# Performance work log

Hardware: AMD Instinct MI355X
Metric: run time of the kernel (lower is better)

## Reference

```python
import jax, jax.numpy as jnp
import numpy as np

N_NODES = 100000
N_EDGES = 1600000
DIMS = [128, 64, 64, 32]  # in -> hidden[0] -> hidden[1] -> out


def setup_inputs() -> dict:
    key = jax.random.key(0)
    ks = jax.random.split(key, 8)
    inp = {
        "features": jax.random.normal(ks[0], (N_NODES, DIMS[0]), dtype=jnp.float32),
        "edge_index": jax.random.randint(ks[1], (2, N_EDGES), 0, N_NODES, dtype=jnp.int32),
    }
    for i in range(3):
        # Glorot-ish init for the GCNConv linear weights; bias zeros (PyG default)
        inp[f"W{i}"] = jax.random.normal(ks[2 + i], (DIMS[i], DIMS[i + 1]), dtype=jnp.float32) / np.sqrt(DIMS[i]).astype(np.float32)
        inp[f"b{i}"] = jnp.zeros((DIMS[i + 1],), dtype=jnp.float32)
    return inp


def _gcn_conv(x, src, dst, norm, W, b, n):
    # PyG GCNConv: linear transform first, then normalized neighbor aggregation, then bias
    x = x @ W                                  # [n, d_out]
    msg = x[src] * norm[:, None]               # gather over edges (+ self loops)
    out = jax.ops.segment_sum(msg, dst, num_segments=n)
    return out + b


def reference(features, edge_index, W0, b0, W1, b1, W2, b2):
    n = features.shape[0]
    # add self loops (GCNConv default add_self_loops=True)
    loop = jnp.arange(n, dtype=edge_index.dtype)
    src = jnp.concatenate([edge_index[0], loop])
    dst = jnp.concatenate([edge_index[1], loop])
    # symmetric normalization: deg from destination (in-degree incl. self loops)
    deg = jax.ops.segment_sum(jnp.ones_like(dst, dtype=features.dtype), dst, num_segments=n)
    dis = jnp.where(deg > 0, jax.lax.rsqrt(jnp.maximum(deg, 1e-12)), 0.0)
    norm = dis[src] * dis[dst]                 # [E + n]

    x = jax.nn.relu(_gcn_conv(features, src, dst, norm, W0, b0, n))
    # dropout(p=0.2) treated as identity (deterministic inference reference)
    x = jax.nn.relu(_gcn_conv(x, src, dst, norm, W1, b1, n))
    x = _gcn_conv(x, src, dst, norm, W2, b2, n)  # last layer: no relu/dropout
    return x
```

## Files before the change

kernel.cpp:

```cpp
#include <hip/hip_runtime.h>
#include <hip/hip_fp16.h>

#define N_NODES 100000
#define N_EDGES 1600000
#define NPB 128
#define NBK ((N_NODES + NPB - 1) / NPB)
#define FBLK 256
#define EPB ((N_EDGES + FBLK - 1) / FBLK)
#define CAP 4096
#define SENT64 100000
#define SENT32 200000

typedef _Float16 h8 __attribute__((ext_vector_type(8)));
typedef float f4v __attribute__((ext_vector_type(4)));


__global__ void __launch_bounds__(256) hist_kernel(const int* __restrict__ dst, int* __restrict__ H) {
    __shared__ int h[NBK];
    for (int i = threadIdx.x; i < NBK; i += 256) h[i] = 0;
    __syncthreads();
    const int e0 = blockIdx.x * EPB;
    const int e1 = min(e0 + EPB, N_EDGES);
    for (int e = e0 + threadIdx.x; e < e1; e += 256) atomicAdd(&h[dst[e] >> 7], 1);
    __syncthreads();
    for (int i = threadIdx.x; i < NBK; i += 256) H[blockIdx.x * NBK + i] = h[i];
}


__global__ void __launch_bounds__(256) colscan_kernel(int* __restrict__ H, int* __restrict__ btot) {
    const int t = blockIdx.x * 256 + threadIdx.x;
    if (t >= NBK) return;
    int run = 0;
    for (int k = 0; k < FBLK; ++k) {
        int idx = k * NBK + t;
        int h = H[idx];
        H[idx] = run;
        run += h;
    }
    btot[t] = run;
}


__global__ void __launch_bounds__(1024) bucketscan_kernel(const int* __restrict__ btot,
                                                          int* __restrict__ bbase, int* __restrict__ bptr) {
    __shared__ int sh[1024];
    const int t = threadIdx.x;
    int v = (t < NBK) ? btot[t] : 0;
    sh[t] = v;
    __syncthreads();
    for (int off = 1; off < 1024; off <<= 1) {
        int u = (t >= off) ? sh[t - off] : 0;
        __syncthreads();
        sh[t] += u;
        __syncthreads();
    }
    if (t < NBK) { int e = sh[t] - v; bbase[t] = e; bptr[t] = e; }
    if (t == 0) bptr[NBK] = N_EDGES;
}


__global__ void __launch_bounds__(256) binfill_kernel(const int* __restrict__ src, const int* __restrict__ dst,
                                                      const int* __restrict__ H, const int* __restrict__ bbase,
                                                      int* __restrict__ tmp) {
    __shared__ int cur[NBK];
    const int k = blockIdx.x;
    for (int i = threadIdx.x; i < NBK; i += 256) cur[i] = H[k * NBK + i] + bbase[i];
    __syncthreads();
    const int e0 = k * EPB;
    const int e1 = min(e0 + EPB, N_EDGES);
    for (int e = e0 + threadIdx.x; e < e1; e += 256) {
        int s = src[e];
        int d = dst[e];
        int pos = atomicAdd(&cur[d >> 7], 1);
        tmp[pos] = s | ((d & (NPB - 1)) << 20);
    }
}


__global__ void __launch_bounds__(256) bucketfin_kernel(const int* __restrict__ tmp, const int* __restrict__ bptr,
                                                        int* __restrict__ esrc, int* __restrict__ rowptr,
                                                        float* __restrict__ dis, int n) {
    __shared__ int buf[CAP];
    __shared__ int cnt[NPB];
    __shared__ int sc[NPB];
    __shared__ int rp[NPB];
    __shared__ int fillc[NPB];
    const int b = blockIdx.x;
    const int d0 = b * NPB;
    const int nd = min(NPB, n - d0);
    const int base = bptr[b], end = bptr[b + 1];
    const int count = end - base;
    const int tid = threadIdx.x;

    for (int i = tid; i < NPB; i += 256) { cnt[i] = 0; fillc[i] = 0; }
    __syncthreads();
    for (int e = base + tid; e < end; e += 256) atomicAdd(&cnt[tmp[e] >> 20], 1);
    __syncthreads();

    if (tid < NPB) sc[tid] = cnt[tid];
    __syncthreads();
    for (int off = 1; off < NPB; off <<= 1) {
        int v = (tid < NPB && tid >= off) ? sc[tid - off] : 0;
        __syncthreads();
        if (tid < NPB) sc[tid] += v;
        __syncthreads();
    }
    if (tid < NPB) {
        int excl = sc[tid] - cnt[tid];
        rp[tid] = excl;
        if (tid < nd) {
            rowptr[d0 + tid] = base + excl;
            dis[d0 + tid] = rsqrtf((float)cnt[tid] + 1.0f);
        }
    }
    if (b == NBK - 1 && tid == 0) rowptr[n] = N_EDGES;
    __syncthreads();

    if (count <= CAP) {
        for (int t = base + tid; t < end; t += 256) {
            int w = tmp[t];
            int ld = w >> 20;
            int pos = rp[ld] + atomicAdd(&fillc[ld], 1);
            buf[pos] = w & 0xFFFFF;
        }
        __syncthreads();
        for (int t = tid; t < count; t += 256) esrc[base + t] = buf[t];
    } else {
        for (int t = base + tid; t < end; t += 256) {
            int w = tmp[t];
            int ld = w >> 20;
            int pos = rp[ld] + atomicAdd(&fillc[ld], 1);
            esrc[base + pos] = w & 0xFFFFF;
        }
    }
}


__global__ void transpose_all_kernel(const float* __restrict__ W0, const float* __restrict__ W1,
                                     const float* __restrict__ W2, __half* __restrict__ wt0,
                                     __half* __restrict__ wt1, __half* __restrict__ wt2,
                                     __half* __restrict__ ys) {
    int i = blockIdx.x * blockDim.x + threadIdx.x;
    if (i < 8192)       { int k = i / 64, c = i % 64;                 wt0[c * 128 + k] = __float2half(W0[i]); }
    else if (i < 12288) { int j = i - 8192;  int k = j / 64, c = j % 64; wt1[c * 64 + k] = __float2half(W1[j]); }
    else if (i < 14336) { int j = i - 12288; int k = j / 32, c = j % 32; wt2[c * 64 + k] = __float2half(W2[j]); }
    else if (i < 14368) { ((int*)(ys + (long)SENT64 * 64))[i - 14336] = 0; }
}


template <typename TIN, int DIN, int DOUT>
__global__ void __launch_bounds__(256) gemm_kernel(const TIN* __restrict__ x,
                                                   const __half* __restrict__ wt16,
                                                   const float* __restrict__ dis,
                                                   __half* __restrict__ ys, int n) {
    constexpr int WS = DIN + 8;
    constexpr int NT = DOUT / 16;
    constexpr int KC = DIN / 32;

    __shared__ _Float16 xls[64 * WS];
    __shared__ _Float16 wls[DOUT * WS];

    const int tid  = threadIdx.x;
    const int row0 = blockIdx.x * 64;

    for (int i = tid; i < DOUT * DIN / 8; i += 256) {
        int c = (i * 8) / DIN, k = (i * 8) % DIN;
        *(int4*)&wls[c * WS + k] = *(const int4*)&wt16[c * DIN + k];
    }
    if constexpr (sizeof(TIN) == 4) {
        for (int i = tid; i < 64 * DIN / 4; i += 256) {
            int r = (i * 4) / DIN, k = (i * 4) % DIN;
            float4 v = make_float4(0.f, 0.f, 0.f, 0.f);
            if (row0 + r < n) v = *(const float4*)&x[(long)(row0 + r) * DIN + k];
            _Float16 h[4] = {(_Float16)v.x, (_Float16)v.y, (_Float16)v.z, (_Float16)v.w};
            *(int2*)&xls[r * WS + k] = *(int2*)h;
        }
    } else {
        for (int i = tid; i < 64 * DIN / 8; i += 256) {
            int r = (i * 8) / DIN, k = (i * 8) % DIN;
            int4 v = make_int4(0, 0, 0, 0);
            if (row0 + r < n) v = *(const int4*)&x[(long)(row0 + r) * DIN + k];
            *(int4*)&xls[r * WS + k] = v;
        }
    }
    __syncthreads();

    const int wave = tid >> 6;
    const int lane = tid & 63;
    const int m16  = lane & 15;
    const int quad = lane >> 4;

    f4v acc[NT];
#pragma unroll
    for (int t = 0; t < NT; ++t) acc[t] = (f4v){0.f, 0.f, 0.f, 0.f};

    const int arow = wave * 16 + m16;
#pragma unroll
    for (int kc = 0; kc < KC; ++kc) {
        h8 a = *(const h8*)&xls[arow * WS + kc * 32 + quad * 8];
#pragma unroll
        for (int t = 0; t < NT; ++t) {
            h8 b = *(const h8*)&wls[(t * 16 + m16) * WS + kc * 32 + quad * 8];
            acc[t] = __builtin_amdgcn_mfma_f32_16x16x32_f16(a, b, acc[t], 0, 0, 0);
        }
    }

    float dsv[4];
    int   lrow[4];
#pragma unroll
    for (int reg = 0; reg < 4; ++reg) {
        lrow[reg] = wave * 16 + quad * 4 + reg;
        int grow  = row0 + lrow[reg];
        dsv[reg]  = (grow < n) ? dis[grow] : 0.f;
    }
    __syncthreads();
    _Float16* stage = xls;
#pragma unroll
    for (int t = 0; t < NT; ++t) {
#pragma unroll
        for (int reg = 0; reg < 4; ++reg)
            stage[lrow[reg] * DOUT + t * 16 + m16] = (_Float16)(acc[t][reg] * dsv[reg]);
    }
    __syncthreads();
    for (int i = tid; i < 64 * DOUT / 8; i += 256) {
        int off = i * 8;
        int r = off / DOUT;
        if (row0 + r < n)
            *(int4*)&ys[(long)row0 * DOUT + off] = *(int4*)&stage[off];
    }
}


__device__ __forceinline__ void acc8(int4 w, float* a) {
    __half2* h = (__half2*)&w;
    float2 f0 = __half22float2(h[0]);
    float2 f1 = __half22float2(h[1]);
    float2 f2 = __half22float2(h[2]);
    float2 f3 = __half22float2(h[3]);
    a[0] += f0.x; a[1] += f0.y; a[2] += f1.x; a[3] += f1.y;
    a[4] += f2.x; a[5] += f2.y; a[6] += f3.x; a[7] += f3.y;
}


__global__ void gather2h_kernel(const int* __restrict__ rowptr, const int* __restrict__ esrc,
                                const __half* __restrict__ ys, const float* __restrict__ dis,
                                const float* __restrict__ b, __half* __restrict__ out, int n) {
    const int node = blockIdx.x * 32 + (threadIdx.x >> 3);
    const int c = (threadIdx.x & 7) * 8;
    if (node >= n) return;

    float a[8];
    {
        int4 sw = *(const int4*)&ys[(long)node * 64 + c];
        __half2* h = (__half2*)&sw;
        float2 f0 = __half22float2(h[0]);
        float2 f1 = __half22float2(h[1]);
        float2 f2 = __half22float2(h[2]);
        float2 f3 = __half22float2(h[3]);
        a[0] = f0.x; a[1] = f0.y; a[2] = f1.x; a[3] = f1.y;
        a[4] = f2.x; a[5] = f2.y; a[6] = f3.x; a[7] = f3.y;
    }

    int k = rowptr[node];
    const int end = rowptr[node + 1];
    for (; k < end; k += 8) {
        int u0 = (k + 0 < end) ? esrc[k + 0] : SENT64;
        int u1 = (k + 1 < end) ? esrc[k + 1] : SENT64;
        int u2 = (k + 2 < end) ? esrc[k + 2] : SENT64;
        int u3 = (k + 3 < end) ? esrc[k + 3] : SENT64;
        int u4 = (k + 4 < end) ? esrc[k + 4] : SENT64;
        int u5 = (k + 5 < end) ? esrc[k + 5] : SENT64;
        int u6 = (k + 6 < end) ? esrc[k + 6] : SENT64;
        int u7 = (k + 7 < end) ? esrc[k + 7] : SENT64;
        int4 w0 = *(const int4*)&ys[(long)u0 * 64 + c];
        int4 w1 = *(const int4*)&ys[(long)u1 * 64 + c];
        int4 w2 = *(const int4*)&ys[(long)u2 * 64 + c];
        int4 w3 = *(const int4*)&ys[(long)u3 * 64 + c];
        int4 w4 = *(const int4*)&ys[(long)u4 * 64 + c];
        int4 w5 = *(const int4*)&ys[(long)u5 * 64 + c];
        int4 w6 = *(const int4*)&ys[(long)u6 * 64 + c];
        int4 w7 = *(const int4*)&ys[(long)u7 * 64 + c];
        acc8(w0, a); acc8(w1, a); acc8(w2, a); acc8(w3, a);
        acc8(w4, a); acc8(w5, a); acc8(w6, a); acc8(w7, a);
    }

    const float di = dis[node];
    __half hv[8];
#pragma unroll
    for (int j = 0; j < 8; ++j)
        hv[j] = __float2half(fmaxf(a[j] * di + b[c + j], 0.0f));
    *(int4*)&out[(long)node * 64 + c] = *(int4*)hv;
}


__global__ void gather4h_kernel(const int* __restrict__ rowptr, const int* __restrict__ esrc,
                                const __half* __restrict__ ys, const float* __restrict__ dis,
                                const float* __restrict__ b, float* __restrict__ out, int n) {
    const int node = blockIdx.x * 64 + (threadIdx.x >> 2);
    const int c = (threadIdx.x & 3) * 8;
    if (node >= n) return;

    float a[8];
    {
        int4 sw = *(const int4*)&ys[(long)node * 32 + c];
        __half2* h = (__half2*)&sw;
        float2 f0 = __half22float2(h[0]);
        float2 f1 = __half22float2(h[1]);
        float2 f2 = __half22float2(h[2]);
        float2 f3 = __half22float2(h[3]);
        a[0] = f0.x; a[1] = f0.y; a[2] = f1.x; a[3] = f1.y;
        a[4] = f2.x; a[5] = f2.y; a[6] = f3.x; a[7] = f3.y;
    }

    int k = rowptr[node];
    const int end = rowptr[node + 1];
    for (; k < end; k += 8) {
        int u0 = (k + 0 < end) ? esrc[k + 0] : SENT32;
        int u1 = (k + 1 < end) ? esrc[k + 1] : SENT32;
        int u2 = (k + 2 < end) ? esrc[k + 2] : SENT32;
        int u3 = (k + 3 < end) ? esrc[k + 3] : SENT32;
        int u4 = (k + 4 < end) ? esrc[k + 4] : SENT32;
        int u5 = (k + 5 < end) ? esrc[k + 5] : SENT32;
        int u6 = (k + 6 < end) ? esrc[k + 6] : SENT32;
        int u7 = (k + 7 < end) ? esrc[k + 7] : SENT32;
        int4 w0 = *(const int4*)&ys[(long)u0 * 32 + c];
        int4 w1 = *(const int4*)&ys[(long)u1 * 32 + c];
        int4 w2 = *(const int4*)&ys[(long)u2 * 32 + c];
        int4 w3 = *(const int4*)&ys[(long)u3 * 32 + c];
        int4 w4 = *(const int4*)&ys[(long)u4 * 32 + c];
        int4 w5 = *(const int4*)&ys[(long)u5 * 32 + c];
        int4 w6 = *(const int4*)&ys[(long)u6 * 32 + c];
        int4 w7 = *(const int4*)&ys[(long)u7 * 32 + c];
        acc8(w0, a); acc8(w1, a); acc8(w2, a); acc8(w3, a);
        acc8(w4, a); acc8(w5, a); acc8(w6, a); acc8(w7, a);
    }

    const float di = dis[node];
    float4 o0, o1;
    o0.x = a[0] * di + b[c + 0];
    o0.y = a[1] * di + b[c + 1];
    o0.z = a[2] * di + b[c + 2];
    o0.w = a[3] * di + b[c + 3];
    o1.x = a[4] * di + b[c + 4];
    o1.y = a[5] * di + b[c + 5];
    o1.z = a[6] * di + b[c + 6];
    o1.w = a[7] * di + b[c + 7];
    *(float4*)&out[(long)node * 32 + c] = o0;
    *(float4*)&out[(long)node * 32 + c + 4] = o1;
}


extern "C" void kernel_launch(void* const* d_in, const int* in_sizes, int n_in,
                              void* d_out, int out_size, void* d_ws, size_t ws_size,
                              hipStream_t stream) {
    const float* features = (const float*)d_in[0];
    const int*   ei       = (const int*)d_in[1];
    const float* W0 = (const float*)d_in[2];
    const float* b0 = (const float*)d_in[3];
    const float* W1 = (const float*)d_in[4];
    const float* b1 = (const float*)d_in[5];
    const float* W2 = (const float*)d_in[6];
    const float* b2 = (const float*)d_in[7];

    const int* src = ei;
    const int* dst = ei + N_EDGES;

    const int n = N_NODES;

    int*    H      = (int*)d_ws;
    int*    btot   = (int*)d_ws + 200704;
    int*    bbase  = (int*)d_ws + 201728;
    int*    bptr   = (int*)d_ws + 202752;
    float*  dis    = (float*)d_ws + 204800;
    int*    rowptr = (int*)d_ws + 335872;
    int*    tmp    = (int*)d_ws + 466944;
    int*    esrc   = (int*)d_ws + 2066944;
    __half* ys     = (__half*)((int*)d_ws + 3666944);
    __half* act    = (__half*)((int*)d_ws + 6866976);
    __half* wt0    = (__half*)((int*)d_ws + 10067008);
    __half* wt1    = (__half*)((int*)d_ws + 10071104);
    __half* wt2    = (__half*)((int*)d_ws + 10073152);
    float*  outf   = (float*)d_out;

    hist_kernel<<<FBLK, 256, 0, stream>>>(dst, H);
    colscan_kernel<<<(NBK + 255) / 256, 256, 0, stream>>>(H, btot);
    bucketscan_kernel<<<1, 1024, 0, stream>>>(btot, bbase, bptr);
    binfill_kernel<<<FBLK, 256, 0, stream>>>(src, dst, H, bbase, tmp);
    bucketfin_kernel<<<NBK, 256, 0, stream>>>(tmp, bptr, esrc, rowptr, dis, n);
    transpose_all_kernel<<<57, 256, 0, stream>>>(W0, W1, W2, wt0, wt1, wt2, ys);

    gemm_kernel<float, 128, 64><<<(n + 63) / 64, 256, 0, stream>>>(features, wt0, dis, ys, n);
    gather2h_kernel<<<(n + 31) / 32, 256, 0, stream>>>(rowptr, esrc, ys, dis, b0, act, n);

    gemm_kernel<__half, 64, 64><<<(n + 63) / 64, 256, 0, stream>>>(act, wt1, dis, ys, n);
    gather2h_kernel<<<(n + 31) / 32, 256, 0, stream>>>(rowptr, esrc, ys, dis, b1, act, n);

    gemm_kernel<__half, 64, 32><<<(n + 63) / 64, 256, 0, stream>>>(act, wt2, dis, ys, n);
    gather4h_kernel<<<(n + 63) / 64, 256, 0, stream>>>(rowptr, esrc, ys, dis, b2, outf, n);
}
```

Measured before the change: 281.2 us.

## Store transformed features column-blocked so gathers sweep one cache-friendly 16-column slab

The GEMM now writes its output in a column-blocked layout (16 halfs per row per block, with rows padded to NROW), and each gather thread pair processes one node across all column blocks in sequence. Each pass over the neighbour list touches only a 3.2MB slab, so it has a better chance of staying in cache than the full row-major feature matrix. The cost is that the neighbour index list is re-read once per column block and each thread does more serial work, with fewer lanes per node.

```diff
diff --git a/kernel.cpp b/kernel.cpp
--- a/kernel.cpp
+++ b/kernel.cpp
@@ -8,8 +8,8 @@
 #define FBLK 256
 #define EPB ((N_EDGES + FBLK - 1) / FBLK)
 #define CAP 4096
-#define SENT64 100000
-#define SENT32 200000
+#define NROW 100032
+#define SENT 100000
 
 typedef _Float16 h8 __attribute__((ext_vector_type(8)));
 typedef float f4v __attribute__((ext_vector_type(4)));
@@ -144,7 +144,11 @@
     if (i < 8192)       { int k = i / 64, c = i % 64;                 wt0[c * 128 + k] = __float2half(W0[i]); }
     else if (i < 12288) { int j = i - 8192;  int k = j / 64, c = j % 64; wt1[c * 64 + k] = __float2half(W1[j]); }
     else if (i < 14336) { int j = i - 12288; int k = j / 32, c = j % 32; wt2[c * 64 + k] = __float2half(W2[j]); }
-    else if (i < 14368) { ((int*)(ys + (long)SENT64 * 64))[i - 14336] = 0; }
+    else if (i < 14368) {
+        int j = i - 14336;
+        int cb = j >> 3, w = j & 7;
+        ((int*)ys)[((long)cb * NROW + SENT) * 8 + w] = 0;
+    }
 }
 
 
@@ -225,8 +229,9 @@
     for (int i = tid; i < 64 * DOUT / 8; i += 256) {
         int off = i * 8;
         int r = off / DOUT;
+        int c = off % DOUT;
         if (row0 + r < n)
-            *(int4*)&ys[(long)row0 * DOUT + off] = *(int4*)&stage[off];
+            *(int4*)&ys[((long)(c >> 4) * NROW + row0 + r) * 16 + (c & 15)] = *(int4*)&stage[off];
     }
 }
 
@@ -242,111 +247,119 @@
 }
 
 
-__global__ void gather2h_kernel(const int* __restrict__ rowptr, const int* __restrict__ esrc,
-                                const __half* __restrict__ ys, const float* __restrict__ dis,
-                                const float* __restrict__ b, __half* __restrict__ out, int n) {
-    const int node = blockIdx.x * 32 + (threadIdx.x >> 3);
-    const int c = (threadIdx.x & 7) * 8;
+__global__ void __launch_bounds__(256) gather2h_kernel(const int* __restrict__ rowptr, const int* __restrict__ esrc,
+                                                       const __half* __restrict__ ys, const float* __restrict__ dis,
+                                                       const float* __restrict__ b, __half* __restrict__ out, int n) {
+    const int node = blockIdx.x * 128 + (threadIdx.x >> 1);
+    const int sel = (threadIdx.x & 1) * 8;
     if (node >= n) return;
 
-    float a[8];
-    {
-        int4 sw = *(const int4*)&ys[(long)node * 64 + c];
-        __half2* h = (__half2*)&sw;
-        float2 f0 = __half22float2(h[0]);
-        float2 f1 = __half22float2(h[1]);
-        float2 f2 = __half22float2(h[2]);
-        float2 f3 = __half22float2(h[3]);
-        a[0] = f0.x; a[1] = f0.y; a[2] = f1.x; a[3] = f1.y;
-        a[4] = f2.x; a[5] = f2.y; a[6] = f3.x; a[7] = f3.y;
-    }
-
-    int k = rowptr[node];
-    const int end = rowptr[node + 1];
-    for (; k < end; k += 8) {
-        int u0 = (k + 0 < end) ? esrc[k + 0] : SENT64;
-        int u1 = (k + 1 < end) ? esrc[k + 1] : SENT64;
-        int u2 = (k + 2 < end) ? esrc[k + 2] : SENT64;
-        int u3 = (k + 3 < end) ? esrc[k + 3] : SENT64;
-        int u4 = (k + 4 < end) ? esrc[k + 4] : SENT64;
-        int u5 = (k + 5 < end) ? esrc[k + 5] : SENT64;
-        int u6 = (k + 6 < end) ? esrc[k + 6] : SENT64;
-        int u7 = (k + 7 < end) ? esrc[k + 7] : SENT64;
-        int4 w0 = *(const int4*)&ys[(long)u0 * 64 + c];
-        int4 w1 = *(const int4*)&ys[(long)u1 * 64 + c];
-        int4 w2 = *(const int4*)&ys[(long)u2 * 64 + c];
-        int4 w3 = *(const int4*)&ys[(long)u3 * 64 + c];
-        int4 w4 = *(const int4*)&ys[(long)u4 * 64 + c];
-        int4 w5 = *(const int4*)&ys[(long)u5 * 64 + c];
-        int4 w6 = *(const int4*)&ys[(long)u6 * 64 + c];
-        int4 w7 = *(const int4*)&ys[(long)u7 * 64 + c];
-        acc8(w0, a); acc8(w1, a); acc8(w2, a); acc8(w3, a);
-        acc8(w4, a); acc8(w5, a); acc8(w6, a); acc8(w7, a);
-    }
-
-    const float di = dis[node];
-    __half hv[8];
-#pragma unroll
-    for (int j = 0; j < 8; ++j)
-        hv[j] = __float2half(fmaxf(a[j] * di + b[c + j], 0.0f));
-    *(int4*)&out[(long)node * 64 + c] = *(int4*)hv;
-}
-
-
-__global__ void gather4h_kernel(const int* __restrict__ rowptr, const int* __restrict__ esrc,
-                                const __half* __restrict__ ys, const float* __restrict__ dis,
-                                const float* __restrict__ b, float* __restrict__ out, int n) {
-    const int node = blockIdx.x * 64 + (threadIdx.x >> 2);
-    const int c = (threadIdx.x & 3) * 8;
+    const float di   = dis[node];
+    const int   kbeg = rowptr[node];
+    const int   end  = rowptr[node + 1];
+
+    for (int cb = 0; cb < 4; ++cb) {
+        const __half* yb = ys + (long)cb * NROW * 16;
+        float a[8];
+        {
+            int4 sw = *(const int4*)&yb[(long)node * 16 + sel];
+            __half2* h = (__half2*)&sw;
+            float2 f0 = __half22float2(h[0]);
+            float2 f1 = __half22float2(h[1]);
+            float2 f2 = __half22float2(h[2]);
+            float2 f3 = __half22float2(h[3]);
+            a[0] = f0.x; a[1] = f0.y; a[2] = f1.x; a[3] = f1.y;
+            a[4] = f2.x; a[5] = f2.y; a[6] = f3.x; a[7] = f3.y;
+        }
+
+        for (int k = kbeg; k < end; k += 8) {
+            int u0 = (k + 0 < end) ? esrc[k + 0] : SENT;
+            int u1 = (k + 1 < end) ? esrc[k + 1] : SENT;
+            int u2 = (k + 2 < end) ? esrc[k + 2] : SENT;
+            int u3 = (k + 3 < end) ? esrc[k + 3] : SENT;
+            int u4 = (k + 4 < end) ? esrc[k + 4] : SENT;
+            int u5 = (k + 5 < end) ? esrc[k + 5] : SENT;
+            int u6 = (k + 6 < end) ? esrc[k + 6] : SENT;
+            int u7 = (k + 7 < end) ? esrc[k + 7] : SENT;
+            int4 w0 = *(const int4*)&yb[(long)u0 * 16 + sel];
+            int4 w1 = *(const int4*)&yb[(long)u1 * 16 + sel];
+            int4 w2 = *(const int4*)&yb[(long)u2 * 16 + sel];
+            int4 w3 = *(const int4*)&yb[(long)u3 * 16 + sel];
+            int4 w4 = *(const int4*)&yb[(long)u4 * 16 + sel];
+            int4 w5 = *(const int4*)&yb[(long)u5 * 16 + sel];
+            int4 w6 = *(const int4*)&yb[(long)u6 * 16 + sel];
+            int4 w7 = *(const int4*)&yb[(long)u7 * 16 + sel];
+            acc8(w0, a); acc8(w1, a); acc8(w2, a); acc8(w3, a);
+            acc8(w4, a); acc8(w5, a); acc8(w6, a); acc8(w7, a);
+        }
+
+        __half hv[8];
+#pragma unroll
+        for (int j = 0; j < 8; ++j)
+            hv[j] = __float2half(fmaxf(a[j] * di + b[cb * 16 + sel + j], 0.0f));
+        *(int4*)&out[(long)node * 64 + cb * 16 + sel] = *(int4*)hv;
+    }
+}
+
+
+__global__ void __launch_bounds__(256) gather4h_kernel(const int* __restrict__ rowptr, const int* __restrict__ esrc,
+                                                       const __half* __restrict__ ys, const float* __restrict__ dis,
+                                                       const float* __restrict__ b, float* __restrict__ out, int n) {
+    const int node = blockIdx.x * 128 + (threadIdx.x >> 1);
+    const int sel = (threadIdx.x & 1) * 8;
     if (node >= n) return;
 
-    float a[8];
-    {
-        int4 sw = *(const int4*)&ys[(long)node * 32 + c];
-        __half2* h = (__half2*)&sw;
-        float2 f0 = __half22float2(h[0]);
-        float2 f1 = __half22float2(h[1]);
-        float2 f2 = __half22float2(h[2]);
-        float2 f3 = __half22float2(h[3]);
-        a[0] = f0.x; a[1] = f0.y; a[2] = f1.x; a[3] = f1.y;
-        a[4] = f2.x; a[5] = f2.y; a[6] = f3.x; a[7] = f3.y;
-    }
-
-    int k = rowptr[node];
-    const int end = rowptr[node + 1];
-    for (; k < end; k += 8) {
-        int u0 = (k + 0 < end) ? esrc[k + 0] : SENT32;
-        int u1 = (k + 1 < end) ? esrc[k + 1] : SENT32;
-        int u2 = (k + 2 < end) ? esrc[k + 2] : SENT32;
-        int u3 = (k + 3 < end) ? esrc[k + 3] : SENT32;
-        int u4 = (k + 4 < end) ? esrc[k + 4] : SENT32;
-        int u5 = (k + 5 < end) ? esrc[k + 5] : SENT32;
-        int u6 = (k + 6 < end) ? esrc[k + 6] : SENT32;
-        int u7 = (k + 7 < end) ? esrc[k + 7] : SENT32;
-        int4 w0 = *(const int4*)&ys[(long)u0 * 32 + c];
-        int4 w1 = *(const int4*)&ys[(long)u1 * 32 + c];
-        int4 w2 = *(const int4*)&ys[(long)u2 * 32 + c];
-        int4 w3 = *(const int4*)&ys[(long)u3 * 32 + c];
-        int4 w4 = *(const int4*)&ys[(long)u4 * 32 + c];
-        int4 w5 = *(const int4*)&ys[(long)u5 * 32 + c];
-        int4 w6 = *(const int4*)&ys[(long)u6 * 32 + c];
-        int4 w7 = *(const int4*)&ys[(long)u7 * 32 + c];
-        acc8(w0, a); acc8(w1, a); acc8(w2, a); acc8(w3, a);
-        acc8(w4, a); acc8(w5, a); acc8(w6, a); acc8(w7, a);
-    }
-
-    const float di = dis[node];
-    float4 o0, o1;
-    o0.x = a[0] * di + b[c + 0];
-    o0.y = a[1] * di + b[c + 1];
-    o0.z = a[2] * di + b[c + 2];
-    o0.w = a[3] * di + b[c + 3];
-    o1.x = a[4] * di + b[c + 4];
-    o1.y = a[5] * di + b[c + 5];
-    o1.z = a[6] * di + b[c + 6];
-    o1.w = a[7] * di + b[c + 7];
-    *(float4*)&out[(long)node * 32 + c] = o0;
-    *(float4*)&out[(long)node * 32 + c + 4] = o1;
+    const float di   = dis[node];
+    const int   kbeg = rowptr[node];
+    const int   end  = rowptr[node + 1];
+
+    for (int cb = 0; cb < 2; ++cb) {
+        const __half* yb = ys + (long)cb * NROW * 16;
+        float a[8];
+        {
+            int4 sw = *(const int4*)&yb[(long)node * 16 + sel];
+            __half2* h = (__half2*)&sw;
+            float2 f0 = __half22float2(h[0]);
+            float2 f1 = __half22float2(h[1]);
+            float2 f2 = __half22float2(h[2]);
+            float2 f3 = __half22float2(h[3]);
+            a[0] = f0.x; a[1] = f0.y; a[2] = f1.x; a[3] = f1.y;
+            a[4] = f2.x; a[5] = f2.y; a[6] = f3.x; a[7] = f3.y;
+        }
+
+        for (int k = kbeg; k < end; k += 8) {
+            int u0 = (k + 0 < end) ? esrc[k + 0] : SENT;
+            int u1 = (k + 1 < end) ? esrc[k + 1] : SENT;
+            int u2 = (k + 2 < end) ? esrc[k + 2] : SENT;
+            int u3 = (k + 3 < end) ? esrc[k + 3] : SENT;
+            int u4 = (k + 4 < end) ? esrc[k + 4] : SENT;
+            int u5 = (k + 5 < end) ? esrc[k + 5] : SENT;
+            int u6 = (k + 6 < end) ? esrc[k + 6] : SENT;
+            int u7 = (k + 7 < end) ? esrc[k + 7] : SENT;
+            int4 w0 = *(const int4*)&yb[(long)u0 * 16 + sel];
+            int4 w1 = *(const int4*)&yb[(long)u1 * 16 + sel];
+            int4 w2 = *(const int4*)&yb[(long)u2 * 16 + sel];
+            int4 w3 = *(const int4*)&yb[(long)u3 * 16 + sel];
+            int4 w4 = *(const int4*)&yb[(long)u4 * 16 + sel];
+            int4 w5 = *(const int4*)&yb[(long)u5 * 16 + sel];
+            int4 w6 = *(const int4*)&yb[(long)u6 * 16 + sel];
+            int4 w7 = *(const int4*)&yb[(long)u7 * 16 + sel];
+            acc8(w0, a); acc8(w1, a); acc8(w2, a); acc8(w3, a);
+            acc8(w4, a); acc8(w5, a); acc8(w6, a); acc8(w7, a);
+        }
+
+        float4 o0, o1;
+        o0.x = a[0] * di + b[cb * 16 + sel + 0];
+        o0.y = a[1] * di + b[cb * 16 + sel + 1];
+        o0.z = a[2] * di + b[cb * 16 + sel + 2];
+        o0.w = a[3] * di + b[cb * 16 + sel + 3];
+        o1.x = a[4] * di + b[cb * 16 + sel + 4];
+        o1.y = a[5] * di + b[cb * 16 + sel + 5];
+        o1.z = a[6] * di + b[cb * 16 + sel + 6];
+        o1.w = a[7] * di + b[cb * 16 + sel + 7];
+        *(float4*)&out[(long)node * 32 + cb * 16 + sel] = o0;
+        *(float4*)&out[(long)node * 32 + cb * 16 + sel + 4] = o1;
+    }
 }
 
 
@@ -376,10 +389,10 @@
     int*    tmp    = (int*)d_ws + 466944;
     int*    esrc   = (int*)d_ws + 2066944;
     __half* ys     = (__half*)((int*)d_ws + 3666944);
-    __half* act    = (__half*)((int*)d_ws + 6866976);
-    __half* wt0    = (__half*)((int*)d_ws + 10067008);
-    __half* wt1    = (__half*)((int*)d_ws + 10071104);
-    __half* wt2    = (__half*)((int*)d_ws + 10073152);
+    __half* act    = (__half*)((int*)d_ws + 6867968);
+    __half* wt0    = (__half*)((int*)d_ws + 10067968);
+    __half* wt1    = (__half*)((int*)d_ws + 10072064);
+    __half* wt2    = (__half*)((int*)d_ws + 10074112);
     float*  outf   = (float*)d_out;
 
     hist_kernel<<<FBLK, 256, 0, stream>>>(dst, H);
@@ -390,11 +403,11 @@
     transpose_all_kernel<<<57, 256, 0, stream>>>(W0, W1, W2, wt0, wt1, wt2, ys);
 
     gemm_kernel<float, 128, 64><<<(n + 63) / 64, 256, 0, stream>>>(features, wt0, dis, ys, n);
-    gather2h_kernel<<<(n + 31) / 32, 256, 0, stream>>>(rowptr, esrc, ys, dis, b0, act, n);
+    gather2h_kernel<<<(n + 127) / 128, 256, 0, stream>>>(rowptr, esrc, ys, dis, b0, act, n);
 
     gemm_kernel<__half, 64, 64><<<(n + 63) / 64, 256, 0, stream>>>(act, wt1, dis, ys, n);
-    gather2h_kernel<<<(n + 31) / 32, 256, 0, stream>>>(rowptr, esrc, ys, dis, b1, act, n);
+    gather2h_kernel<<<(n + 127) / 128, 256, 0, stream>>>(rowptr, esrc, ys, dis, b1, act, n);
 
     gemm_kernel<__half, 64, 32><<<(n + 63) / 64, 256, 0, stream>>>(act, wt2, dis, ys, n);
-    gather4h_kernel<<<(n + 63) / 64, 256, 0, stream>>>(rowptr, esrc, ys, dis, b2, outf, n);
-}
+    gather4h_kernel<<<(n + 127) / 128, 256, 0, stream>>>(rowptr, esrc, ys, dis, b2, outf, n);
+}
```

After: 360.9 us. 1.28x slower.
